# Optimization experiments

Measured on AMD Instinct MI355X. Metric: run time of the kernel, lower is better.

Reference implementation:

```python
import jax, jax.numpy as jnp
import numpy as np

HEADS = 16
DIM_HEAD = 64
SCALE = DIM_HEAD ** -0.5

def setup_inputs() -> dict:
    key = jax.random.key(0)
    k1, k2, k3 = jax.random.split(key, 3)
    dim = HEADS * DIM_HEAD  # 1024
    x = jax.random.normal(k1, (2, 4096, dim), dtype=jnp.float32)
    w_qkv = jax.random.normal(k2, (dim, 3 * dim), dtype=jnp.float32) * (dim ** -0.5)
    w_out = jax.random.normal(k3, (dim, dim), dtype=jnp.float32) * (dim ** -0.5)
    return {"x": x, "w_qkv": w_qkv, "w_out": w_out}

def reference(x, w_qkv, w_out):
    b, n, dim = x.shape
    qkv = x @ w_qkv  # (b, n, 3*h*d)
    qkv = qkv.reshape(b, n, 3, HEADS, DIM_HEAD)
    q, k, v = (qkv[:, :, 0], qkv[:, :, 1], qkv[:, :, 2])  # (b, n, h, d)
    q = jnp.swapaxes(q, 1, 2) * SCALE  # (b, h, n, d)
    k = jnp.swapaxes(k, 1, 2)
    v = jnp.swapaxes(v, 1, 2)
    sim = jnp.einsum('bhid,bhjd->bhij', q, k)
    mask_value = -jnp.finfo(sim.dtype).max
    causal_mask = jnp.triu(jnp.ones((n, n), dtype=bool), k=1)
    sim = jnp.where(causal_mask, mask_value, sim)
    attn = jax.nn.softmax(sim, axis=-1)
    out = jnp.einsum('bhij,bhjd->bhid', attn, v)
    out = jnp.swapaxes(out, 1, 2).reshape(b, n, HEADS * DIM_HEAD)
    return out @ w_out
```

## Files before the change

### kernel.cpp

```cpp
#include <hip/hip_runtime.h>
#include <stdint.h>
#include <stddef.h>

typedef __attribute__((ext_vector_type(8))) short bf16x8;
typedef __attribute__((ext_vector_type(4))) short bf16x4;
typedef __attribute__((ext_vector_type(4))) float f32x4;
typedef __attribute__((ext_vector_type(4))) unsigned short u16x4;
typedef __attribute__((ext_vector_type(2))) unsigned int u32x2;

#define BATCH 2
#define SEQ 4096
#define NHEADS 16
#define DHEAD 64
#define DIM 1024
#define MTOT 8192
#define N1 3072
#define NEGINF -3.0e4f
#define QSCALE 0.18033688f

__device__ __forceinline__ unsigned short f2bf(float f) {
  union { float f; unsigned u; } x; x.f = f;
  unsigned r = x.u + 0x7fffu + ((x.u >> 16) & 1u);
  return (unsigned short)(r >> 16);
}

__device__ __forceinline__ float fexp2(float x) {
  return __builtin_amdgcn_exp2f(x);
}

__device__ __forceinline__ unsigned pk_bf16(float a, float b) {
  unsigned d;
  asm("v_cvt_pk_bf16_f32 %0, %1, %2" : "=v"(d) : "v"(a), "v"(b));
  return d;
}

__device__ __forceinline__ void gload_lds16(const void* g, void* l) {
  __builtin_amdgcn_global_load_lds(
      (const __attribute__((address_space(1))) void*)g,
      (__attribute__((address_space(3))) void*)l, 16, 0, 0);
}

__global__ __launch_bounds__(256) void cvt_f2b(const float* __restrict__ in,
                                               unsigned short* __restrict__ out,
                                               int n4) {
  int i = blockIdx.x * 256 + threadIdx.x;
  if (i < n4) {
    f32x4 v = ((const f32x4*)in)[i];
    u16x4 o;
#pragma unroll
    for (int j = 0; j < 4; j++) o[j] = f2bf(v[j]);
    ((u16x4*)out)[i] = o;
  }
}

__global__ void transpose_cvt(const float* __restrict__ in,
                              unsigned short* __restrict__ out, int R, int C) {
  __shared__ unsigned short t[32][33];
  int tx = threadIdx.x, ty = threadIdx.y;
  int c0 = blockIdx.x * 32, r0 = blockIdx.y * 32;
#pragma unroll
  for (int i = 0; i < 4; i++)
    t[ty + i * 8][tx] = f2bf(in[(size_t)(r0 + ty + i * 8) * C + c0 + tx]);
  __syncthreads();
#pragma unroll
  for (int i = 0; i < 4; i++)
    out[(size_t)(c0 + ty + i * 8) * R + r0 + tx] = t[tx][ty + i * 8];
}

template <int MODE>
__global__ __launch_bounds__(256) void gemm_bt(
    const unsigned short* __restrict__ A,
    const unsigned short* __restrict__ Bt,
    unsigned short* __restrict__ O0,
    unsigned short* __restrict__ O1,
    unsigned short* __restrict__ O2,
    float* __restrict__ Of,
    int N, int K) {
  __shared__ unsigned short Asl[128][32];
  __shared__ unsigned short Bsl[128][32];
  const int tid = threadIdx.x;
  const int lane = tid & 63, wv = tid >> 6;
  const int wr = wv >> 1, wc = wv & 1;
  const int m0 = blockIdx.x * 128, n0 = blockIdx.y * 128;
  const int lrow = lane >> 2, lcol = (lane & 3) * 8;
  const int fr = lane & 15, kc8 = (lane >> 4) * 8;
  f32x4 acc[4][4] = {};
  for (int k0 = 0; k0 < K; k0 += 32) {
#pragma unroll
    for (int c = 0; c < 2; c++) {
      int r = wv * 32 + c * 16 + lrow;
      gload_lds16(&A[(size_t)(m0 + r) * K + k0 + lcol], &Asl[wv * 32 + c * 16][0]);
      gload_lds16(&Bt[(size_t)(n0 + r) * K + k0 + lcol], &Bsl[wv * 32 + c * 16][0]);
    }
    __syncthreads();
    bf16x8 af[4], bfr[4];
#pragma unroll
    for (int i = 0; i < 4; i++)
      af[i] = *(const bf16x8*)&Asl[wr * 64 + i * 16 + fr][kc8];
#pragma unroll
    for (int j = 0; j < 4; j++)
      bfr[j] = *(const bf16x8*)&Bsl[wc * 64 + j * 16 + fr][kc8];
#pragma unroll
    for (int i = 0; i < 4; i++)
#pragma unroll
      for (int j = 0; j < 4; j++)
        acc[i][j] = __builtin_amdgcn_mfma_f32_16x16x32_bf16(af[i], bfr[j], acc[i][j], 0, 0, 0);
    __syncthreads();
  }
  const int rq = (lane >> 4) * 4;
  if (MODE == 0) {
    const int wblk = n0 >> 10;
#pragma unroll
    for (int i = 0; i < 4; i++) {
      int rowb = m0 + wr * 64 + i * 16 + rq;
      int b = rowb >> 12, n = rowb & 4095;
      size_t bhb = (size_t)b * NHEADS;
#pragma unroll
      for (int j = 0; j < 4; j++) {
        int col = n0 + wc * 64 + j * 16 + fr;
        int rem = col & 1023, h = rem >> 6, d = rem & 63;
        size_t bh = bhb + h;
        if (wblk == 0) {
#pragma unroll
          for (int r = 0; r < 4; r++)
            O0[(bh * SEQ + n + r) * DHEAD + d] = f2bf(acc[i][j][r] * QSCALE);
        } else if (wblk == 1) {
#pragma unroll
          for (int r = 0; r < 4; r++)
            O1[(bh * SEQ + n + r) * DHEAD + d] = f2bf(acc[i][j][r]);
        } else {
          u16x4 pk;
#pragma unroll
          for (int r = 0; r < 4; r++) pk[r] = f2bf(acc[i][j][r]);
          *(u16x4*)&O2[(bh * DHEAD + d) * SEQ + n] = pk;
        }
      }
    }
  } else {
#pragma unroll
    for (int i = 0; i < 4; i++)
#pragma unroll
      for (int j = 0; j < 4; j++)
#pragma unroll
        for (int r = 0; r < 4; r++) {
          int row = m0 + wr * 64 + i * 16 + rq + r;
          int col = n0 + wc * 64 + j * 16 + fr;
          Of[(size_t)row * N + col] = acc[i][j][r];
        }
  }
}

__device__ __forceinline__ void attn_tile3(
    int qt, const unsigned short* __restrict__ Qp,
    const unsigned short* __restrict__ Kp,
    const unsigned short* __restrict__ Vp,
    unsigned short* __restrict__ AOp,
    unsigned short* __restrict__ Kl,
    unsigned short* __restrict__ Vl,
    int lane, int wv) {
  const int fr = lane & 15, g = lane >> 4;
  const int kc8 = g * 8, rq = g * 4;
  const int sw = fr & 7;
  const int gh = g >> 1, glo = g & 1;
  const int q0 = qt * 64;
  const int srl = lane >> 3;
  const int jl = lane & 7;

  bf16x8 qf0 = *(const bf16x8*)&Qp[(size_t)(q0 + wv * 16 + fr) * DHEAD + kc8];
  bf16x8 qf1 = *(const bf16x8*)&Qp[(size_t)(q0 + wv * 16 + fr) * DHEAD + 32 + kc8];

  f32x4 oacc[4] = {};
  float lrow = 0.f;

#pragma unroll
  for (int c = 0; c < 2; c++) {
    int seg = wv * 2 + c;
    int r = seg * 8 + srl;
    int j = jl ^ (r & 7);
    gload_lds16(&Kp[(size_t)r * DHEAD + j * 8], Kl + seg * 512);
    gload_lds16(&Vp[(size_t)r * SEQ + j * 8], Vl + seg * 512);
  }
  __syncthreads();

  int cur = 0;
  for (int kt = 0; kt <= qt; kt++) {
    const int ktn = (kt < qt) ? kt + 1 : qt;
    unsigned short* Kc = Kl + cur * 4096;
    unsigned short* Vc = Vl + cur * 4096;
    unsigned short* Kn = Kl + (cur ^ 1) * 4096;
    unsigned short* Vn = Vl + (cur ^ 1) * 4096;
#pragma unroll
    for (int c = 0; c < 2; c++) {
      int seg = wv * 2 + c;
      int r = seg * 8 + srl;
      int j = jl ^ (r & 7);
      gload_lds16(&Kp[(size_t)(ktn * 64 + r) * DHEAD + j * 8], Kn + seg * 512);
      gload_lds16(&Vp[(size_t)r * SEQ + ktn * 64 + j * 8], Vn + seg * 512);
    }
    f32x4 sv[4];
    __builtin_amdgcn_s_setprio(1);
#pragma unroll
    for (int cb = 0; cb < 4; cb++) {
      bf16x8 kf0 = *(const bf16x8*)&Kc[(cb * 16 + fr) * 64 + ((g ^ sw) << 3)];
      bf16x8 kf1 = *(const bf16x8*)&Kc[(cb * 16 + fr) * 64 + (((4 + g) ^ sw) << 3)];
      f32x4 z = {};
      z = __builtin_amdgcn_mfma_f32_16x16x32_bf16(kf0, qf0, z, 0, 0, 0);
      sv[cb] = __builtin_amdgcn_mfma_f32_16x16x32_bf16(kf1, qf1, z, 0, 0, 0);
    }
    __builtin_amdgcn_s_setprio(0);
    if (kt == qt) {
#pragma unroll
      for (int cb = 0; cb < 4; cb++)
#pragma unroll
        for (int r = 0; r < 4; r++)
          if (cb * 16 + rq + r > wv * 16 + fr) sv[cb][r] = NEGINF;
    }
    float p[4][4];
#pragma unroll
    for (int cb = 0; cb < 4; cb++)
#pragma unroll
      for (int r = 0; r < 4; r++)
        p[cb][r] = fexp2(sv[cb][r]);
    float t0 = (p[0][0] + p[0][1]) + (p[0][2] + p[0][3]);
    float t1 = (p[1][0] + p[1][1]) + (p[1][2] + p[1][3]);
    float t2 = (p[2][0] + p[2][1]) + (p[2][2] + p[2][3]);
    float t3 = (p[3][0] + p[3][1]) + (p[3][2] + p[3][3]);
    lrow += (t0 + t1) + (t2 + t3);
    bf16x4 pw[4];
#pragma unroll
    for (int cb = 0; cb < 4; cb++) {
      u32x2 w;
      w[0] = pk_bf16(p[cb][0], p[cb][1]);
      w[1] = pk_bf16(p[cb][2], p[cb][3]);
      pw[cb] = *(bf16x4*)&w;
    }
    __builtin_amdgcn_s_setprio(1);
#pragma unroll
    for (int db = 0; db < 4; db++) {
      const int vbase = (db * 16 + fr) * 64;
#pragma unroll
      for (int cb = 0; cb < 4; cb++) {
        bf16x4 vf = *(const bf16x4*)&Vc[vbase + (((cb * 2 + gh) ^ sw) << 3) + (glo << 2)];
        oacc[db] = __builtin_amdgcn_mfma_f32_16x16x16bf16_1k(pw[cb], vf, oacc[db], 0, 0, 0);
      }
    }
    __builtin_amdgcn_s_setprio(0);
    __syncthreads();
    cur ^= 1;
  }

  lrow += __shfl_xor(lrow, 16, 64);
  lrow += __shfl_xor(lrow, 32, 64);
  float i0 = __builtin_amdgcn_rcpf(__shfl(lrow, rq + 0, 64));
  float i1 = __builtin_amdgcn_rcpf(__shfl(lrow, rq + 1, 64));
  float i2 = __builtin_amdgcn_rcpf(__shfl(lrow, rq + 2, 64));
  float i3 = __builtin_amdgcn_rcpf(__shfl(lrow, rq + 3, 64));
#pragma unroll
  for (int db = 0; db < 4; db++) {
    int nb = q0 + wv * 16 + rq;
    int d = db * 16 + fr;
    AOp[(size_t)(nb + 0) * DIM + d] = f2bf(oacc[db][0] * i0);
    AOp[(size_t)(nb + 1) * DIM + d] = f2bf(oacc[db][1] * i1);
    AOp[(size_t)(nb + 2) * DIM + d] = f2bf(oacc[db][2] * i2);
    AOp[(size_t)(nb + 3) * DIM + d] = f2bf(oacc[db][3] * i3);
  }
}

__global__ __launch_bounds__(256, 4) void attn_causal(
    const unsigned short* __restrict__ Q,
    const unsigned short* __restrict__ Kb,
    const unsigned short* __restrict__ Vt,
    unsigned short* __restrict__ AO) {
  const int id = blockIdx.x;
  const int xcd = id & 7, t = id >> 3;
  const int pi = t & 31, bq = t >> 5;
  const int bh = xcd * 4 + bq;
  const int tid = threadIdx.x, lane = tid & 63, wv = tid >> 6;

  const unsigned short* Qp = Q + (size_t)bh * SEQ * DHEAD;
  const unsigned short* Kp = Kb + (size_t)bh * SEQ * DHEAD;
  const unsigned short* Vp = Vt + (size_t)bh * DHEAD * SEQ;
  const int b = bh >> 4, h = bh & 15;
  unsigned short* AOp = AO + (size_t)b * SEQ * DIM + h * DHEAD;

  __shared__ unsigned short Kl[2][4096];
  __shared__ unsigned short Vl[2][4096];

  attn_tile3(pi, Qp, Kp, Vp, AOp, &Kl[0][0], &Vl[0][0], lane, wv);
  attn_tile3(63 - pi, Qp, Kp, Vp, AOp, &Kl[0][0], &Vl[0][0], lane, wv);
}

extern "C" void kernel_launch(void* const* d_in, const int* in_sizes, int n_in,
                              void* d_out, int out_size, void* d_ws, size_t ws_size,
                              hipStream_t stream) {
  const float* x    = (const float*)d_in[0];
  const float* wqkv = (const float*)d_in[1];
  const float* wout = (const float*)d_in[2];
  float* out = (float*)d_out;

  unsigned short* ws = (unsigned short*)d_ws;
  unsigned short* xb = ws;
  unsigned short* ao = ws;
  unsigned short* wqkv_t = ws + (size_t)MTOT * DIM;
  unsigned short* wout_t = wqkv_t + (size_t)N1 * DIM;
  unsigned short* qb = wout_t + (size_t)DIM * DIM;
  unsigned short* kb = qb + (size_t)BATCH * NHEADS * SEQ * DHEAD;
  unsigned short* vt = kb + (size_t)BATCH * NHEADS * SEQ * DHEAD;

  int n4 = (MTOT * DIM) / 4;
  hipLaunchKernelGGL(cvt_f2b, dim3(n4 / 256), dim3(256), 0, stream, x, xb, n4);

  dim3 tb(32, 8);
  hipLaunchKernelGGL(transpose_cvt, dim3(N1 / 32, DIM / 32), tb, 0, stream,
                     wqkv, wqkv_t, DIM, N1);
  hipLaunchKernelGGL(transpose_cvt, dim3(DIM / 32, DIM / 32), tb, 0, stream,
                     wout, wout_t, DIM, DIM);

  hipLaunchKernelGGL((gemm_bt<0>), dim3(MTOT / 128, N1 / 128), dim3(256), 0, stream,
                     xb, wqkv_t, qb, kb, vt, nullptr, N1, DIM);

  hipLaunchKernelGGL(attn_causal, dim3(32 * 32), dim3(256), 0, stream,
                     qb, kb, vt, ao);

  hipLaunchKernelGGL((gemm_bt<1>), dim3(MTOT / 128, DIM / 128), dim3(256), 0, stream,
                     ao, wout_t, nullptr, nullptr, nullptr, out, DIM, DIM);
}
```

Measured before the change: 227.1 us.

## Process paired causal query tiles in one pass sharing K/V loads

Each attention block previously ran its two query tiles (pi and 63-pi) one after the other, loading the K/V tiles twice. The two tiles now run in a single loop over key tiles: every K/V tile is loaded to LDS once and feeds both query tiles' MFMAs, with the shorter tile gated by a doA flag. Block-to-(head, tile) mapping also alternates direction per head. This cuts global/LDS traffic and barriers, at the cost of roughly doubling accumulator and score registers, which may lower occupancy under the launch bounds.

```diff
diff --git a/kernel.cpp b/kernel.cpp
--- a/kernel.cpp
+++ b/kernel.cpp
@@ -150,8 +150,8 @@
   }
 }
 
-__device__ __forceinline__ void attn_tile3(
-    int qt, const unsigned short* __restrict__ Qp,
+__device__ __forceinline__ void attn_dual(
+    int ta, int tb, const unsigned short* __restrict__ Qp,
     const unsigned short* __restrict__ Kp,
     const unsigned short* __restrict__ Vp,
     unsigned short* __restrict__ AOp,
@@ -162,15 +162,17 @@
   const int kc8 = g * 8, rq = g * 4;
   const int sw = fr & 7;
   const int gh = g >> 1, glo = g & 1;
-  const int q0 = qt * 64;
+  const int q0A = ta * 64, q0B = tb * 64;
   const int srl = lane >> 3;
   const int jl = lane & 7;
 
-  bf16x8 qf0 = *(const bf16x8*)&Qp[(size_t)(q0 + wv * 16 + fr) * DHEAD + kc8];
-  bf16x8 qf1 = *(const bf16x8*)&Qp[(size_t)(q0 + wv * 16 + fr) * DHEAD + 32 + kc8];
-
-  f32x4 oacc[4] = {};
-  float lrow = 0.f;
+  bf16x8 qA0 = *(const bf16x8*)&Qp[(size_t)(q0A + wv * 16 + fr) * DHEAD + kc8];
+  bf16x8 qA1 = *(const bf16x8*)&Qp[(size_t)(q0A + wv * 16 + fr) * DHEAD + 32 + kc8];
+  bf16x8 qB0 = *(const bf16x8*)&Qp[(size_t)(q0B + wv * 16 + fr) * DHEAD + kc8];
+  bf16x8 qB1 = *(const bf16x8*)&Qp[(size_t)(q0B + wv * 16 + fr) * DHEAD + 32 + kc8];
+
+  f32x4 oA[4] = {}, oB[4] = {};
+  float lA = 0.f, lB = 0.f;
 
 #pragma unroll
   for (int c = 0; c < 2; c++) {
@@ -183,8 +185,9 @@
   __syncthreads();
 
   int cur = 0;
-  for (int kt = 0; kt <= qt; kt++) {
-    const int ktn = (kt < qt) ? kt + 1 : qt;
+  for (int kt = 0; kt <= tb; kt++) {
+    const int ktn = (kt < tb) ? kt + 1 : tb;
+    const bool doA = (kt <= ta);
     unsigned short* Kc = Kl + cur * 4096;
     unsigned short* Vc = Vl + cur * 4096;
     unsigned short* Kn = Kl + (cur ^ 1) * 4096;
@@ -197,42 +200,76 @@
       gload_lds16(&Kp[(size_t)(ktn * 64 + r) * DHEAD + j * 8], Kn + seg * 512);
       gload_lds16(&Vp[(size_t)r * SEQ + ktn * 64 + j * 8], Vn + seg * 512);
     }
-    f32x4 sv[4];
+    f32x4 svA[4], svB[4];
     __builtin_amdgcn_s_setprio(1);
 #pragma unroll
     for (int cb = 0; cb < 4; cb++) {
       bf16x8 kf0 = *(const bf16x8*)&Kc[(cb * 16 + fr) * 64 + ((g ^ sw) << 3)];
       bf16x8 kf1 = *(const bf16x8*)&Kc[(cb * 16 + fr) * 64 + (((4 + g) ^ sw) << 3)];
-      f32x4 z = {};
-      z = __builtin_amdgcn_mfma_f32_16x16x32_bf16(kf0, qf0, z, 0, 0, 0);
-      sv[cb] = __builtin_amdgcn_mfma_f32_16x16x32_bf16(kf1, qf1, z, 0, 0, 0);
+      f32x4 zb = {};
+      zb = __builtin_amdgcn_mfma_f32_16x16x32_bf16(kf0, qB0, zb, 0, 0, 0);
+      svB[cb] = __builtin_amdgcn_mfma_f32_16x16x32_bf16(kf1, qB1, zb, 0, 0, 0);
+      if (doA) {
+        f32x4 za = {};
+        za = __builtin_amdgcn_mfma_f32_16x16x32_bf16(kf0, qA0, za, 0, 0, 0);
+        svA[cb] = __builtin_amdgcn_mfma_f32_16x16x32_bf16(kf1, qA1, za, 0, 0, 0);
+      }
     }
     __builtin_amdgcn_s_setprio(0);
-    if (kt == qt) {
+    if (kt == ta) {
 #pragma unroll
       for (int cb = 0; cb < 4; cb++)
 #pragma unroll
         for (int r = 0; r < 4; r++)
-          if (cb * 16 + rq + r > wv * 16 + fr) sv[cb][r] = NEGINF;
-    }
-    float p[4][4];
-#pragma unroll
-    for (int cb = 0; cb < 4; cb++)
-#pragma unroll
-      for (int r = 0; r < 4; r++)
-        p[cb][r] = fexp2(sv[cb][r]);
-    float t0 = (p[0][0] + p[0][1]) + (p[0][2] + p[0][3]);
-    float t1 = (p[1][0] + p[1][1]) + (p[1][2] + p[1][3]);
-    float t2 = (p[2][0] + p[2][1]) + (p[2][2] + p[2][3]);
-    float t3 = (p[3][0] + p[3][1]) + (p[3][2] + p[3][3]);
-    lrow += (t0 + t1) + (t2 + t3);
-    bf16x4 pw[4];
-#pragma unroll
-    for (int cb = 0; cb < 4; cb++) {
-      u32x2 w;
-      w[0] = pk_bf16(p[cb][0], p[cb][1]);
-      w[1] = pk_bf16(p[cb][2], p[cb][3]);
-      pw[cb] = *(bf16x4*)&w;
+          if (cb * 16 + rq + r > wv * 16 + fr) svA[cb][r] = NEGINF;
+    }
+    if (kt == tb) {
+#pragma unroll
+      for (int cb = 0; cb < 4; cb++)
+#pragma unroll
+        for (int r = 0; r < 4; r++)
+          if (cb * 16 + rq + r > wv * 16 + fr) svB[cb][r] = NEGINF;
+    }
+    bf16x4 pwA[4], pwB[4];
+    if (doA) {
+      float p[4][4];
+#pragma unroll
+      for (int cb = 0; cb < 4; cb++)
+#pragma unroll
+        for (int r = 0; r < 4; r++)
+          p[cb][r] = fexp2(svA[cb][r]);
+      float t0 = (p[0][0] + p[0][1]) + (p[0][2] + p[0][3]);
+      float t1 = (p[1][0] + p[1][1]) + (p[1][2] + p[1][3]);
+      float t2 = (p[2][0] + p[2][1]) + (p[2][2] + p[2][3]);
+      float t3 = (p[3][0] + p[3][1]) + (p[3][2] + p[3][3]);
+      lA += (t0 + t1) + (t2 + t3);
+#pragma unroll
+      for (int cb = 0; cb < 4; cb++) {
+        u32x2 w;
+        w[0] = pk_bf16(p[cb][0], p[cb][1]);
+        w[1] = pk_bf16(p[cb][2], p[cb][3]);
+        pwA[cb] = *(bf16x4*)&w;
+      }
+    }
+    {
+      float p[4][4];
+#pragma unroll
+      for (int cb = 0; cb < 4; cb++)
+#pragma unroll
+        for (int r = 0; r < 4; r++)
+          p[cb][r] = fexp2(svB[cb][r]);
+      float t0 = (p[0][0] + p[0][1]) + (p[0][2] + p[0][3]);
+      float t1 = (p[1][0] + p[1][1]) + (p[1][2] + p[1][3]);
+      float t2 = (p[2][0] + p[2][1]) + (p[2][2] + p[2][3]);
+      float t3 = (p[3][0] + p[3][1]) + (p[3][2] + p[3][3]);
+      lB += (t0 + t1) + (t2 + t3);
+#pragma unroll
+      for (int cb = 0; cb < 4; cb++) {
+        u32x2 w;
+        w[0] = pk_bf16(p[cb][0], p[cb][1]);
+        w[1] = pk_bf16(p[cb][2], p[cb][3]);
+        pwB[cb] = *(bf16x4*)&w;
+      }
     }
     __builtin_amdgcn_s_setprio(1);
 #pragma unroll
@@ -241,7 +278,9 @@
 #pragma unroll
       for (int cb = 0; cb < 4; cb++) {
         bf16x4 vf = *(const bf16x4*)&Vc[vbase + (((cb * 2 + gh) ^ sw) << 3) + (glo << 2)];
-        oacc[db] = __builtin_amdgcn_mfma_f32_16x16x16bf16_1k(pw[cb], vf, oacc[db], 0, 0, 0);
+        oB[db] = __builtin_amdgcn_mfma_f32_16x16x16bf16_1k(pwB[cb], vf, oB[db], 0, 0, 0);
+        if (doA)
+          oA[db] = __builtin_amdgcn_mfma_f32_16x16x16bf16_1k(pwA[cb], vf, oA[db], 0, 0, 0);
       }
     }
     __builtin_amdgcn_s_setprio(0);
@@ -249,20 +288,26 @@
     cur ^= 1;
   }
 
-  lrow += __shfl_xor(lrow, 16, 64);
-  lrow += __shfl_xor(lrow, 32, 64);
-  float i0 = __builtin_amdgcn_rcpf(__shfl(lrow, rq + 0, 64));
-  float i1 = __builtin_amdgcn_rcpf(__shfl(lrow, rq + 1, 64));
-  float i2 = __builtin_amdgcn_rcpf(__shfl(lrow, rq + 2, 64));
-  float i3 = __builtin_amdgcn_rcpf(__shfl(lrow, rq + 3, 64));
-#pragma unroll
-  for (int db = 0; db < 4; db++) {
-    int nb = q0 + wv * 16 + rq;
-    int d = db * 16 + fr;
-    AOp[(size_t)(nb + 0) * DIM + d] = f2bf(oacc[db][0] * i0);
-    AOp[(size_t)(nb + 1) * DIM + d] = f2bf(oacc[db][1] * i1);
-    AOp[(size_t)(nb + 2) * DIM + d] = f2bf(oacc[db][2] * i2);
-    AOp[(size_t)(nb + 3) * DIM + d] = f2bf(oacc[db][3] * i3);
+#pragma unroll
+  for (int s = 0; s < 2; s++) {
+    float lrow = s ? lB : lA;
+    const f32x4* oacc = s ? oB : oA;
+    int q0 = s ? q0B : q0A;
+    lrow += __shfl_xor(lrow, 16, 64);
+    lrow += __shfl_xor(lrow, 32, 64);
+    float i0 = __builtin_amdgcn_rcpf(__shfl(lrow, rq + 0, 64));
+    float i1 = __builtin_amdgcn_rcpf(__shfl(lrow, rq + 1, 64));
+    float i2 = __builtin_amdgcn_rcpf(__shfl(lrow, rq + 2, 64));
+    float i3 = __builtin_amdgcn_rcpf(__shfl(lrow, rq + 3, 64));
+#pragma unroll
+    for (int db = 0; db < 4; db++) {
+      int nb = q0 + wv * 16 + rq;
+      int d = db * 16 + fr;
+      AOp[(size_t)(nb + 0) * DIM + d] = f2bf(oacc[db][0] * i0);
+      AOp[(size_t)(nb + 1) * DIM + d] = f2bf(oacc[db][1] * i1);
+      AOp[(size_t)(nb + 2) * DIM + d] = f2bf(oacc[db][2] * i2);
+      AOp[(size_t)(nb + 3) * DIM + d] = f2bf(oacc[db][3] * i3);
+    }
   }
 }
 
@@ -272,9 +317,12 @@
     const unsigned short* __restrict__ Vt,
     unsigned short* __restrict__ AO) {
   const int id = blockIdx.x;
-  const int xcd = id & 7, t = id >> 3;
-  const int pi = t & 31, bq = t >> 5;
-  const int bh = xcd * 4 + bq;
+  const int xcd = id & 7;
+  const int inner = id >> 3;
+  const int c = inner & 31;
+  const int k = inner >> 5;
+  const int pi = (k & 1) ? (31 - c) : c;
+  const int bh = xcd * 4 + k;
   const int tid = threadIdx.x, lane = tid & 63, wv = tid >> 6;
 
   const unsigned short* Qp = Q + (size_t)bh * SEQ * DHEAD;
@@ -286,8 +334,7 @@
   __shared__ unsigned short Kl[2][4096];
   __shared__ unsigned short Vl[2][4096];
 
-  attn_tile3(pi, Qp, Kp, Vp, AOp, &Kl[0][0], &Vl[0][0], lane, wv);
-  attn_tile3(63 - pi, Qp, Kp, Vp, AOp, &Kl[0][0], &Vl[0][0], lane, wv);
+  attn_dual(pi, 63 - pi, Qp, Kp, Vp, AOp, &Kl[0][0], &Vl[0][0], lane, wv);
 }
 
 extern "C" void kernel_launch(void* const* d_in, const int* in_sizes, int n_in,
@@ -319,7 +366,7 @@
   hipLaunchKernelGGL((gemm_bt<0>), dim3(MTOT / 128, N1 / 128), dim3(256), 0, stream,
                      xb, wqkv_t, qb, kb, vt, nullptr, N1, DIM);
 
-  hipLaunchKernelGGL(attn_causal, dim3(32 * 32), dim3(256), 0, stream,
+  hipLaunchKernelGGL(attn_causal, dim3(1024), dim3(256), 0, stream,
                      qb, kb, vt, ao);
 
   hipLaunchKernelGGL((gemm_bt<1>), dim3(MTOT / 128, DIM / 128), dim3(256), 0, stream,
```

Measured after the change: 235.3 us. 3.6% more time.

## Process 128-row query tiles per block so each K/V tile feeds two subtiles

Applied to the files above, without the earlier changes.

The attention kernel now gives each block one 128-query tile, with each wave handling two 16-row subtiles, instead of two paired 64-row tiles processed one after the other. Every K/V tile loaded into LDS is reused across twice as many query rows, which halves LDS and global K/V traffic per unit of work and keeps MFMA issue denser. Causal balancing moves into a new block-index mapping that pairs short and long tiles across blocks instead of inside one block. The cost is more registers, with the occupancy hint lowered from 4 to 3, and coarser blocks whose lengths vary more.

```diff
diff --git a/kernel.cpp b/kernel.cpp
--- a/kernel.cpp
+++ b/kernel.cpp
@@ -150,8 +150,8 @@
   }
 }
 
-__device__ __forceinline__ void attn_tile3(
-    int qt, const unsigned short* __restrict__ Qp,
+__device__ __forceinline__ void attn_tile2s(
+    int tq, const unsigned short* __restrict__ Qp,
     const unsigned short* __restrict__ Kp,
     const unsigned short* __restrict__ Vp,
     unsigned short* __restrict__ AOp,
@@ -162,15 +162,20 @@
   const int kc8 = g * 8, rq = g * 4;
   const int sw = fr & 7;
   const int gh = g >> 1, glo = g & 1;
-  const int q0 = qt * 64;
+  const int q0 = tq * 128;
   const int srl = lane >> 3;
   const int jl = lane & 7;
-
-  bf16x8 qf0 = *(const bf16x8*)&Qp[(size_t)(q0 + wv * 16 + fr) * DHEAD + kc8];
-  bf16x8 qf1 = *(const bf16x8*)&Qp[(size_t)(q0 + wv * 16 + fr) * DHEAD + 32 + kc8];
-
-  f32x4 oacc[4] = {};
-  float lrow = 0.f;
+  const int ktmax = 2 * tq + 1;
+
+  bf16x8 qf[2][2];
+#pragma unroll
+  for (int s = 0; s < 2; s++)
+#pragma unroll
+    for (int c = 0; c < 2; c++)
+      qf[s][c] = *(const bf16x8*)&Qp[(size_t)(q0 + wv * 32 + s * 16 + fr) * DHEAD + c * 32 + kc8];
+
+  f32x4 oacc[2][4] = {};
+  float lrow[2] = {0.f, 0.f};
 
 #pragma unroll
   for (int c = 0; c < 2; c++) {
@@ -183,8 +188,8 @@
   __syncthreads();
 
   int cur = 0;
-  for (int kt = 0; kt <= qt; kt++) {
-    const int ktn = (kt < qt) ? kt + 1 : qt;
+  for (int kt = 0; kt <= ktmax; kt++) {
+    const int ktn = (kt < ktmax) ? kt + 1 : ktmax;
     unsigned short* Kc = Kl + cur * 4096;
     unsigned short* Vc = Vl + cur * 4096;
     unsigned short* Kn = Kl + (cur ^ 1) * 4096;
@@ -197,42 +202,52 @@
       gload_lds16(&Kp[(size_t)(ktn * 64 + r) * DHEAD + j * 8], Kn + seg * 512);
       gload_lds16(&Vp[(size_t)r * SEQ + ktn * 64 + j * 8], Vn + seg * 512);
     }
-    f32x4 sv[4];
+    f32x4 sv[2][4];
     __builtin_amdgcn_s_setprio(1);
 #pragma unroll
     for (int cb = 0; cb < 4; cb++) {
       bf16x8 kf0 = *(const bf16x8*)&Kc[(cb * 16 + fr) * 64 + ((g ^ sw) << 3)];
       bf16x8 kf1 = *(const bf16x8*)&Kc[(cb * 16 + fr) * 64 + (((4 + g) ^ sw) << 3)];
-      f32x4 z = {};
-      z = __builtin_amdgcn_mfma_f32_16x16x32_bf16(kf0, qf0, z, 0, 0, 0);
-      sv[cb] = __builtin_amdgcn_mfma_f32_16x16x32_bf16(kf1, qf1, z, 0, 0, 0);
+      f32x4 z0 = {};
+      z0 = __builtin_amdgcn_mfma_f32_16x16x32_bf16(kf0, qf[0][0], z0, 0, 0, 0);
+      sv[0][cb] = __builtin_amdgcn_mfma_f32_16x16x32_bf16(kf1, qf[0][1], z0, 0, 0, 0);
+      f32x4 z1 = {};
+      z1 = __builtin_amdgcn_mfma_f32_16x16x32_bf16(kf0, qf[1][0], z1, 0, 0, 0);
+      sv[1][cb] = __builtin_amdgcn_mfma_f32_16x16x32_bf16(kf1, qf[1][1], z1, 0, 0, 0);
     }
     __builtin_amdgcn_s_setprio(0);
-    if (kt == qt) {
+    if (kt >= 2 * tq) {
+      const int delta = (kt - 2 * tq) << 6;
+#pragma unroll
+      for (int s = 0; s < 2; s++)
+#pragma unroll
+        for (int cb = 0; cb < 4; cb++)
+#pragma unroll
+          for (int r = 0; r < 4; r++)
+            if (cb * 16 + rq + r + delta > wv * 32 + s * 16 + fr)
+              sv[s][cb][r] = NEGINF;
+    }
+    bf16x4 pw[2][4];
+#pragma unroll
+    for (int s = 0; s < 2; s++) {
+      float p[4][4];
 #pragma unroll
       for (int cb = 0; cb < 4; cb++)
 #pragma unroll
         for (int r = 0; r < 4; r++)
-          if (cb * 16 + rq + r > wv * 16 + fr) sv[cb][r] = NEGINF;
-    }
-    float p[4][4];
-#pragma unroll
-    for (int cb = 0; cb < 4; cb++)
-#pragma unroll
-      for (int r = 0; r < 4; r++)
-        p[cb][r] = fexp2(sv[cb][r]);
-    float t0 = (p[0][0] + p[0][1]) + (p[0][2] + p[0][3]);
-    float t1 = (p[1][0] + p[1][1]) + (p[1][2] + p[1][3]);
-    float t2 = (p[2][0] + p[2][1]) + (p[2][2] + p[2][3]);
-    float t3 = (p[3][0] + p[3][1]) + (p[3][2] + p[3][3]);
-    lrow += (t0 + t1) + (t2 + t3);
-    bf16x4 pw[4];
-#pragma unroll
-    for (int cb = 0; cb < 4; cb++) {
-      u32x2 w;
-      w[0] = pk_bf16(p[cb][0], p[cb][1]);
-      w[1] = pk_bf16(p[cb][2], p[cb][3]);
-      pw[cb] = *(bf16x4*)&w;
+          p[cb][r] = fexp2(sv[s][cb][r]);
+      float t0 = (p[0][0] + p[0][1]) + (p[0][2] + p[0][3]);
+      float t1 = (p[1][0] + p[1][1]) + (p[1][2] + p[1][3]);
+      float t2 = (p[2][0] + p[2][1]) + (p[2][2] + p[2][3]);
+      float t3 = (p[3][0] + p[3][1]) + (p[3][2] + p[3][3]);
+      lrow[s] += (t0 + t1) + (t2 + t3);
+#pragma unroll
+      for (int cb = 0; cb < 4; cb++) {
+        u32x2 w;
+        w[0] = pk_bf16(p[cb][0], p[cb][1]);
+        w[1] = pk_bf16(p[cb][2], p[cb][3]);
+        pw[s][cb] = *(bf16x4*)&w;
+      }
     }
     __builtin_amdgcn_s_setprio(1);
 #pragma unroll
@@ -241,7 +256,8 @@
 #pragma unroll
       for (int cb = 0; cb < 4; cb++) {
         bf16x4 vf = *(const bf16x4*)&Vc[vbase + (((cb * 2 + gh) ^ sw) << 3) + (glo << 2)];
-        oacc[db] = __builtin_amdgcn_mfma_f32_16x16x16bf16_1k(pw[cb], vf, oacc[db], 0, 0, 0);
+        oacc[0][db] = __builtin_amdgcn_mfma_f32_16x16x16bf16_1k(pw[0][cb], vf, oacc[0][db], 0, 0, 0);
+        oacc[1][db] = __builtin_amdgcn_mfma_f32_16x16x16bf16_1k(pw[1][cb], vf, oacc[1][db], 0, 0, 0);
       }
     }
     __builtin_amdgcn_s_setprio(0);
@@ -249,32 +265,42 @@
     cur ^= 1;
   }
 
-  lrow += __shfl_xor(lrow, 16, 64);
-  lrow += __shfl_xor(lrow, 32, 64);
-  float i0 = __builtin_amdgcn_rcpf(__shfl(lrow, rq + 0, 64));
-  float i1 = __builtin_amdgcn_rcpf(__shfl(lrow, rq + 1, 64));
-  float i2 = __builtin_amdgcn_rcpf(__shfl(lrow, rq + 2, 64));
-  float i3 = __builtin_amdgcn_rcpf(__shfl(lrow, rq + 3, 64));
-#pragma unroll
-  for (int db = 0; db < 4; db++) {
-    int nb = q0 + wv * 16 + rq;
-    int d = db * 16 + fr;
-    AOp[(size_t)(nb + 0) * DIM + d] = f2bf(oacc[db][0] * i0);
-    AOp[(size_t)(nb + 1) * DIM + d] = f2bf(oacc[db][1] * i1);
-    AOp[(size_t)(nb + 2) * DIM + d] = f2bf(oacc[db][2] * i2);
-    AOp[(size_t)(nb + 3) * DIM + d] = f2bf(oacc[db][3] * i3);
-  }
-}
-
-__global__ __launch_bounds__(256, 4) void attn_causal(
+#pragma unroll
+  for (int s = 0; s < 2; s++) {
+    float lr = lrow[s];
+    lr += __shfl_xor(lr, 16, 64);
+    lr += __shfl_xor(lr, 32, 64);
+    float i0 = __builtin_amdgcn_rcpf(__shfl(lr, rq + 0, 64));
+    float i1 = __builtin_amdgcn_rcpf(__shfl(lr, rq + 1, 64));
+    float i2 = __builtin_amdgcn_rcpf(__shfl(lr, rq + 2, 64));
+    float i3 = __builtin_amdgcn_rcpf(__shfl(lr, rq + 3, 64));
+    int nb = q0 + wv * 32 + s * 16 + rq;
+#pragma unroll
+    for (int db = 0; db < 4; db++) {
+      int d = db * 16 + fr;
+      AOp[(size_t)(nb + 0) * DIM + d] = f2bf(oacc[s][db][0] * i0);
+      AOp[(size_t)(nb + 1) * DIM + d] = f2bf(oacc[s][db][1] * i1);
+      AOp[(size_t)(nb + 2) * DIM + d] = f2bf(oacc[s][db][2] * i2);
+      AOp[(size_t)(nb + 3) * DIM + d] = f2bf(oacc[s][db][3] * i3);
+    }
+  }
+}
+
+__global__ __launch_bounds__(256, 3) void attn_causal(
     const unsigned short* __restrict__ Q,
     const unsigned short* __restrict__ Kb,
     const unsigned short* __restrict__ Vt,
     unsigned short* __restrict__ AO) {
   const int id = blockIdx.x;
-  const int xcd = id & 7, t = id >> 3;
-  const int pi = t & 31, bq = t >> 5;
-  const int bh = xcd * 4 + bq;
+  const int xcd = id & 7;
+  const int inner = id >> 3;
+  const int cl = inner & 15;
+  const int ch = (inner >> 4) & 1;
+  const int r0 = (inner >> 5) & 1;
+  const int r1 = (inner >> 6) & 1;
+  const int w = cl + 16 * r1;
+  const int tq = r0 ? (31 - w) : w;
+  const int bh = xcd * 4 + (ch + 2 * r0);
   const int tid = threadIdx.x, lane = tid & 63, wv = tid >> 6;
 
   const unsigned short* Qp = Q + (size_t)bh * SEQ * DHEAD;
@@ -286,8 +312,7 @@
   __shared__ unsigned short Kl[2][4096];
   __shared__ unsigned short Vl[2][4096];
 
-  attn_tile3(pi, Qp, Kp, Vp, AOp, &Kl[0][0], &Vl[0][0], lane, wv);
-  attn_tile3(63 - pi, Qp, Kp, Vp, AOp, &Kl[0][0], &Vl[0][0], lane, wv);
+  attn_tile2s(tq, Qp, Kp, Vp, AOp, &Kl[0][0], &Vl[0][0], lane, wv);
 }
 
 extern "C" void kernel_launch(void* const* d_in, const int* in_sizes, int n_in,
@@ -319,7 +344,7 @@
   hipLaunchKernelGGL((gemm_bt<0>), dim3(MTOT / 128, N1 / 128), dim3(256), 0, stream,
                      xb, wqkv_t, qb, kb, vt, nullptr, N1, DIM);
 
-  hipLaunchKernelGGL(attn_causal, dim3(32 * 32), dim3(256), 0, stream,
+  hipLaunchKernelGGL(attn_causal, dim3(1024), dim3(256), 0, stream,
                      qb, kb, vt, ao);
 
   hipLaunchKernelGGL((gemm_bt<1>), dim3(MTOT / 128, DIM / 128), dim3(256), 0, stream,
```

Result: no change. 226.1 us (-0.5%).
